# Performance work log

Measured on AMD Instinct MI355X. Metric: run time of the kernel, lower is better.

Reference implementation:

```python
import jax, jax.numpy as jnp
import numpy as np

M = 128  # split point: first M units use max-plus, rest use min-plus

def setup_inputs() -> dict:
    key = jax.random.key(0)
    k1, k2 = jax.random.split(key)
    x = jax.random.normal(k1, (2048, 512), dtype=jnp.float32)   # (batch, features_in)
    w = jax.random.normal(k2, (512, 256), dtype=jnp.float32)    # (features_in, units)
    return {"x": x, "w": w}

def reference(x, w):
    # Tropical (max/min-plus) pseudo-matmul.
    # s[b, f, u] = x[b, f] + w[f, u]; reduce over f.
    s_max = x[:, :, None] + w[None, :, :M]          # (batch, f, M)
    s_min = x[:, :, None] + w[None, :, M:]          # (batch, f, units-M)
    hv = jnp.max(s_max, axis=1)                     # (batch, M)
    hw = jnp.min(s_min, axis=1)                     # (batch, units-M)
    return jnp.concatenate([hv, hw], axis=1)        # linear activation = identity
```

## Files before the change

### kernel.cpp

```cpp
#include <hip/hip_runtime.h>
#include <math.h>


#define FEAT  512
#define UNITS 256
#define BR    8
#define NW    8
#define KW    128
#define NS    (KW / 4)
#define LDSZ  24576

__device__ __forceinline__ float max3f(float a, float b, float c) {
    return fmaxf(fmaxf(a, b), c);
}
__device__ __forceinline__ float min3f(float a, float b, float c) {
    return fminf(fminf(a, b), c);
}

__device__ __forceinline__ void load_xstep(const float* __restrict__ xp, int s,
                                           float4* __restrict__ xb) {
    #pragma unroll
    for (int r = 0; r < BR; ++r)
        xb[r] = *(const float4*)(xp + r * FEAT + s * 4);
}

__device__ __forceinline__ void load_wstep(const float* __restrict__ wp, int s,
                                           float2* __restrict__ wb) {
    #pragma unroll
    for (int j = 0; j < 4; ++j)
        wb[j] = *(const float2*)(wp + (size_t)(s * 4 + j) * UNITS);
}

template<bool ISMAX>
__device__ __forceinline__ void compute_step(const float4* __restrict__ xb,
                                             const float2* __restrict__ wq,
                                             float2* __restrict__ acc) {
    #pragma unroll
    for (int r = 0; r < BR; ++r) {
        const float4 a = xb[r];
        const float t0x = a.x + wq[0].x, t0y = a.x + wq[0].y;
        const float t1x = a.y + wq[1].x, t1y = a.y + wq[1].y;
        const float t2x = a.z + wq[2].x, t2y = a.z + wq[2].y;
        const float t3x = a.w + wq[3].x, t3y = a.w + wq[3].y;
        float2 A = acc[r];
        if (ISMAX) {
            A.x = max3f(A.x, t0x, t1x);  A.x = max3f(A.x, t2x, t3x);
            A.y = max3f(A.y, t0y, t1y);  A.y = max3f(A.y, t2y, t3y);
        } else {
            A.x = min3f(A.x, t0x, t1x);  A.x = min3f(A.x, t2x, t3x);
            A.y = min3f(A.y, t0y, t1y);  A.y = min3f(A.y, t2y, t3y);
        }
        acc[r] = A;
    }
}

template<bool ISMAX>
__device__ __forceinline__ void main_loop(const float* __restrict__ xp,
                                          const float* __restrict__ wp,
                                          float2* __restrict__ acc) {
    float4 xA[BR], xB[BR];
    float2 wA[4], wB[4];
    load_xstep(xp, 0, xA);
    load_wstep(wp, 0, wA);
    #pragma unroll 1
    for (int s = 0; s < NS; s += 2) {
        load_xstep(xp, s + 1, xB);
        load_wstep(wp, s + 1, wB);
        compute_step<ISMAX>(xA, wA, acc);
        if (s + 2 < NS) {
            load_xstep(xp, s + 2, xA);
            load_wstep(wp, s + 2, wA);
        }
        compute_step<ISMAX>(xB, wB, acc);
    }
}

__global__ __launch_bounds__(512)
__attribute__((amdgpu_waves_per_eu(2, 2)))
void tropical_kernel(const float* __restrict__ x,
                     const float* __restrict__ w,
                     float* __restrict__ out) {
    __shared__ float lds[LDSZ];
    const int tid  = threadIdx.x;
    const int lane = tid & 63;
    const int wv   = __builtin_amdgcn_readfirstlane(tid >> 6);
    const int ks   = (wv & 3) * KW;
    const int half = wv >> 2;
    const int u0   = lane * 2;
    const int row0 = blockIdx.x * BR;

    const float* xp = x + (size_t)row0 * FEAT + ks;
    const float* wp = w + (size_t)ks * UNITS + half * 128 + u0;

    float2 acc[BR];
    const float init = half ? __builtin_inff() : -__builtin_inff();
    #pragma unroll
    for (int r = 0; r < BR; ++r)
        acc[r] = make_float2(init, init);

    if (half == 0) main_loop<true >(xp, wp, acc);
    else           main_loop<false>(xp, wp, acc);

    #pragma unroll
    for (int r = 0; r < BR; ++r)
        *(float2*)&lds[(wv * BR + r) * 128 + u0] = acc[r];
    __syncthreads();

    const int r  = tid >> 6;
    const int u4 = (tid & 63) * 4;
    const int hh = u4 >> 7;
    const int uo = u4 & 127;
    const float4 p0 = *(const float4*)&lds[((hh * 4 + 0) * BR + r) * 128 + uo];
    const float4 p1 = *(const float4*)&lds[((hh * 4 + 1) * BR + r) * 128 + uo];
    const float4 p2 = *(const float4*)&lds[((hh * 4 + 2) * BR + r) * 128 + uo];
    const float4 p3 = *(const float4*)&lds[((hh * 4 + 3) * BR + r) * 128 + uo];
    float4 v;
    if (hh == 0) {
        v.x = fmaxf(fmaxf(p0.x, p1.x), fmaxf(p2.x, p3.x));
        v.y = fmaxf(fmaxf(p0.y, p1.y), fmaxf(p2.y, p3.y));
        v.z = fmaxf(fmaxf(p0.z, p1.z), fmaxf(p2.z, p3.z));
        v.w = fmaxf(fmaxf(p0.w, p1.w), fmaxf(p2.w, p3.w));
    } else {
        v.x = fminf(fminf(p0.x, p1.x), fminf(p2.x, p3.x));
        v.y = fminf(fminf(p0.y, p1.y), fminf(p2.y, p3.y));
        v.z = fminf(fminf(p0.z, p1.z), fminf(p2.z, p3.z));
        v.w = fminf(fminf(p0.w, p1.w), fminf(p2.w, p3.w));
    }
    *(float4*)&out[(size_t)(row0 + r) * UNITS + u4] = v;
}

extern "C" void kernel_launch(void* const* d_in, const int* in_sizes, int n_in,
                              void* d_out, int out_size, void* d_ws, size_t ws_size,
                              hipStream_t stream) {
    const float* x = (const float*)d_in[0];
    const float* w = (const float*)d_in[1];
    float* out = (float*)d_out;

    tropical_kernel<<<dim3(2048 / BR), dim3(512), 0, stream>>>(x, w, out);
}
```

Before: 71.45 us.

## Split feature reduction over 8 waves per half and load x via scalar constant path

```diff
diff --git a/kernel.cpp b/kernel.cpp
--- a/kernel.cpp
+++ b/kernel.cpp
@@ -5,10 +5,12 @@
 #define FEAT  512
 #define UNITS 256
 #define BR    8
-#define NW    8
-#define KW    128
+#define NW    16
+#define KW    64
 #define NS    (KW / 4)
 #define LDSZ  24576
+
+typedef __attribute__((address_space(4))) const float cfloat;
 
 __device__ __forceinline__ float max3f(float a, float b, float c) {
     return fmaxf(fmaxf(a, b), c);
@@ -17,11 +19,16 @@
     return fminf(fminf(a, b), c);
 }
 
-__device__ __forceinline__ void load_xstep(const float* __restrict__ xp, int s,
+__device__ __forceinline__ void load_xstep(cfloat* __restrict__ xp, int s,
                                            float4* __restrict__ xb) {
     #pragma unroll
-    for (int r = 0; r < BR; ++r)
-        xb[r] = *(const float4*)(xp + r * FEAT + s * 4);
+    for (int r = 0; r < BR; ++r) {
+        const int o = r * FEAT + s * 4;
+        xb[r].x = xp[o + 0];
+        xb[r].y = xp[o + 1];
+        xb[r].z = xp[o + 2];
+        xb[r].w = xp[o + 3];
+    }
 }
 
 __device__ __forceinline__ void load_wstep(const float* __restrict__ wp, int s,
@@ -55,7 +62,7 @@
 }
 
 template<bool ISMAX>
-__device__ __forceinline__ void main_loop(const float* __restrict__ xp,
+__device__ __forceinline__ void main_loop(cfloat* __restrict__ xp,
                                           const float* __restrict__ wp,
                                           float2* __restrict__ acc) {
     float4 xA[BR], xB[BR];
@@ -75,8 +82,8 @@
     }
 }
 
-__global__ __launch_bounds__(512)
-__attribute__((amdgpu_waves_per_eu(2, 2)))
+__global__ __launch_bounds__(1024)
+__attribute__((amdgpu_waves_per_eu(4, 4)))
 void tropical_kernel(const float* __restrict__ x,
                      const float* __restrict__ w,
                      float* __restrict__ out) {
@@ -84,12 +91,13 @@
     const int tid  = threadIdx.x;
     const int lane = tid & 63;
     const int wv   = __builtin_amdgcn_readfirstlane(tid >> 6);
-    const int ks   = (wv & 3) * KW;
-    const int half = wv >> 2;
+    const int kslice = wv & 7;
+    const int half   = wv >> 3;
+    const int ks   = kslice * KW;
     const int u0   = lane * 2;
     const int row0 = blockIdx.x * BR;
 
-    const float* xp = x + (size_t)row0 * FEAT + ks;
+    cfloat* xp = (cfloat*)(unsigned long long)(x + (size_t)row0 * FEAT + ks);
     const float* wp = w + (size_t)ks * UNITS + half * 128 + u0;
 
     float2 acc[BR];
@@ -106,27 +114,18 @@
         *(float2*)&lds[(wv * BR + r) * 128 + u0] = acc[r];
     __syncthreads();
 
-    const int r  = tid >> 6;
-    const int u4 = (tid & 63) * 4;
-    const int hh = u4 >> 7;
-    const int uo = u4 & 127;
-    const float4 p0 = *(const float4*)&lds[((hh * 4 + 0) * BR + r) * 128 + uo];
-    const float4 p1 = *(const float4*)&lds[((hh * 4 + 1) * BR + r) * 128 + uo];
-    const float4 p2 = *(const float4*)&lds[((hh * 4 + 2) * BR + r) * 128 + uo];
-    const float4 p3 = *(const float4*)&lds[((hh * 4 + 3) * BR + r) * 128 + uo];
-    float4 v;
-    if (hh == 0) {
-        v.x = fmaxf(fmaxf(p0.x, p1.x), fmaxf(p2.x, p3.x));
-        v.y = fmaxf(fmaxf(p0.y, p1.y), fmaxf(p2.y, p3.y));
-        v.z = fmaxf(fmaxf(p0.z, p1.z), fmaxf(p2.z, p3.z));
-        v.w = fmaxf(fmaxf(p0.w, p1.w), fmaxf(p2.w, p3.w));
-    } else {
-        v.x = fminf(fminf(p0.x, p1.x), fminf(p2.x, p3.x));
-        v.y = fminf(fminf(p0.y, p1.y), fminf(p2.y, p3.y));
-        v.z = fminf(fminf(p0.z, p1.z), fminf(p2.z, p3.z));
-        v.w = fminf(fminf(p0.w, p1.w), fminf(p2.w, p3.w));
+    const int r  = tid >> 7;
+    const int j2 = tid & 127;
+    const int hh = j2 >> 6;
+    const int uo = (j2 & 63) * 2;
+    float2 v = *(const float2*)&lds[((hh * 8 + 0) * BR + r) * 128 + uo];
+    #pragma unroll
+    for (int j = 1; j < 8; ++j) {
+        const float2 p = *(const float2*)&lds[((hh * 8 + j) * BR + r) * 128 + uo];
+        if (hh == 0) { v.x = fmaxf(v.x, p.x); v.y = fmaxf(v.y, p.y); }
+        else         { v.x = fminf(v.x, p.x); v.y = fminf(v.y, p.y); }
     }
-    *(float4*)&out[(size_t)(row0 + r) * UNITS + u4] = v;
+    *(float2*)&out[(size_t)(row0 + r) * UNITS + hh * 128 + uo] = v;
 }
 
 extern "C" void kernel_launch(void* const* d_in, const int* in_sizes, int n_in,
@@ -136,5 +135,5 @@
     const float* w = (const float*)d_in[1];
     float* out = (float*)d_out;
 
-    tropical_kernel<<<dim3(2048 / BR), dim3(512), 0, stream>>>(x, w, out);
+    tropical_kernel<<<dim3(2048 / BR), dim3(1024), 0, stream>>>(x, w, out);
 }
```

New measurement: 68.07 us. 4.7% less time.
